# Performance work log

Measured on AMD Instinct MI355X. Metric: run time of the kernel, lower is better.

The kernel has to match this reference:

```python
import jax, jax.numpy as jnp
import numpy as np

B, S, D_IN, D_OUT, H = 2, 2048, 1024, 1024, 16
HD = D_OUT // H


def setup_inputs() -> dict:
    key = jax.random.key(0)
    ks = jax.random.split(key, 6)
    x = jax.random.normal(ks[0], (B, S, D_IN), jnp.float32)
    Wq = jax.random.normal(ks[1], (D_IN, D_OUT), jnp.float32) * 0.02
    Wk = jax.random.normal(ks[2], (D_IN, D_OUT), jnp.float32) * 0.02
    Wv = jax.random.normal(ks[3], (D_IN, D_OUT), jnp.float32) * 0.02
    Wo = jax.random.normal(ks[4], (D_OUT, D_OUT), jnp.float32) * 0.02
    bo = jax.random.normal(ks[5], (D_OUT,), jnp.float32) * 0.02
    return {"x": x, "Wq": Wq, "Wk": Wk, "Wv": Wv, "Wo": Wo, "bo": bo}


def reference(x, Wq, Wk, Wv, Wo, bo):
    b, s, _ = x.shape

    def to_heads(t):  # [b, s, d_out] -> [b, h, s, hd]
        return t.reshape(b, s, H, HD).transpose(0, 2, 1, 3)

    Q = to_heads(x @ Wq)
    K = to_heads(x @ Wk)
    V = to_heads(x @ Wv)

    scale = 1.0 / jnp.sqrt(jnp.asarray(HD, x.dtype))
    scores = jnp.einsum("bhqd,bhkd->bhqk", Q, K) * scale
    causal_mask = jnp.triu(jnp.ones((s, s), dtype=bool), k=1)  # True above diag
    scores = jnp.where(causal_mask, jnp.asarray(-1e6, scores.dtype), scores)
    weights = jax.nn.softmax(scores, axis=-1)  # dropout p=0.0 -> identity
    attn = jnp.einsum("bhqk,bhkd->bhqd", weights, V)  # [b, h, s, hd]
    # Faithful to source: reshape [b,h,s,hd] -> [b,s,d_out] WITHOUT head transpose-back
    attn = attn.reshape(b, s, D_OUT)
    return attn @ Wo + bo
```

## Files before the change

### kernel.cpp

```cpp
#include <hip/hip_runtime.h>
#include <stdint.h>


typedef unsigned short u16;
typedef __attribute__((ext_vector_type(8))) short bf16x8;
typedef __attribute__((ext_vector_type(4))) float f32x4;

#define MFMA_BF16(a, b, c) __builtin_amdgcn_mfma_f32_16x16x32_bf16((a), (b), (c), 0, 0, 0)
#define QSCALE 0.18033688011112042f

__device__ __forceinline__ u16 f2bf(float f) {
  union { float f; unsigned int u; } x; x.f = f;
  unsigned int r = x.u + 0x7fffu + ((x.u >> 16) & 1u);
  return (u16)(r >> 16);
}
__device__ __forceinline__ bf16x8 pack8(float4 a, float4 b) {
  bf16x8 r;
  r[0] = (short)f2bf(a.x); r[1] = (short)f2bf(a.y);
  r[2] = (short)f2bf(a.z); r[3] = (short)f2bf(a.w);
  r[4] = (short)f2bf(b.x); r[5] = (short)f2bf(b.y);
  r[6] = (short)f2bf(b.z); r[7] = (short)f2bf(b.w);
  return r;
}
__device__ __forceinline__ void gload_lds16(const u16* g, u16* l) {
  __builtin_amdgcn_global_load_lds((__attribute__((address_space(1))) void*)g,
                                   (__attribute__((address_space(3))) void*)l, 16, 0, 0);
}

template <int CPR>
__device__ __forceinline__ int sw_off(int r, int c) {
  return (r * CPR + (c ^ (r & (CPR - 1)))) * 8;
}

__global__ __launch_bounds__(256) void x_to_bf16(const float* __restrict__ x,
                                                 u16* __restrict__ xb) {
  const size_t i = ((size_t)blockIdx.x * 256 + threadIdx.x) * 8;
  const float4 a = *(const float4*)&x[i];
  const float4 b = *(const float4*)&x[i + 4];
  *(bf16x8*)&xb[i] = pack8(a, b);
}

__global__ void transpose_cols(const float* __restrict__ W0, const float* __restrict__ W1,
                               const float* __restrict__ W2, u16* __restrict__ T,
                               int h0, int hsx64) {
  __shared__ u16 t[32][33];
  const int j0 = blockIdx.x * 32;
  const int g = j0 / hsx64;
  const float* W = (g == 0) ? W0 : (g == 1) ? W1 : W2;
  const int wc0 = h0 * 64 + (j0 % hsx64);
  const int k0 = blockIdx.y * 32;
  t[threadIdx.y][threadIdx.x] =
      f2bf(W[(size_t)(k0 + threadIdx.y) * 1024 + wc0 + threadIdx.x]);
  __syncthreads();
  T[(size_t)(j0 + threadIdx.y) * 1024 + k0 + threadIdx.x] = t[threadIdx.x][threadIdx.y];
}

template <int MODE, int AF32>
__global__ __launch_bounds__(256, 2) void gemm_bt(
    const void* __restrict__ Av, const u16* __restrict__ BT,
    void* __restrict__ C0v, u16* __restrict__ C1, u16* __restrict__ C2,
    const float* __restrict__ bias, int M, int N, int K, int hs, int h0) {
  __shared__ __align__(16) u16 lsA[128 * 32];
  __shared__ __align__(16) u16 lsB[128 * 32];
  const int tid = threadIdx.x, lane = tid & 63, wv = tid >> 6;
  const int quad = lane >> 4, l16 = lane & 15;
  const int m0 = blockIdx.y * 128, n0 = blockIdx.x * 128;
  const int wm = (wv >> 1) * 64, wn = (wv & 1) * 64;
  const int hs64 = hs * 64;
  f32x4 acc[4][4] = {};

  for (int k0 = 0; k0 < K; k0 += 32) {
    if constexpr (AF32) {
      bf16x8 va[2], vb[2];
#pragma unroll
      for (int c = 0; c < 2; ++c) {
        const int P = c * 256 + tid, r = P >> 2, cc = P & 3;
        const float* Af = (const float*)Av;
        const float4 a0 = *(const float4*)&Af[(size_t)(m0 + r) * K + k0 + cc * 8];
        const float4 a1 = *(const float4*)&Af[(size_t)(m0 + r) * K + k0 + cc * 8 + 4];
        va[c] = pack8(a0, a1);
        vb[c] = *(const bf16x8*)&BT[(size_t)(n0 + r) * K + k0 + cc * 8];
      }
      __syncthreads();
#pragma unroll
      for (int c = 0; c < 2; ++c) {
        const int P = c * 256 + tid, r = P >> 2, cc = P & 3;
        *(bf16x8*)&lsA[sw_off<4>(r, cc)] = va[c];
        *(bf16x8*)&lsB[sw_off<4>(r, cc)] = vb[c];
      }
      __syncthreads();
    } else {
      __syncthreads();
#pragma unroll
      for (int c = 0; c < 2; ++c) {
        const int P = c * 256 + tid, r = P >> 2;
        const int gcol = ((P & 3) ^ (r & 3)) * 8;
        gload_lds16((const u16*)Av + (size_t)(m0 + r) * K + k0 + gcol,
                    &lsA[(size_t)(c * 256 + wv * 64) * 8]);
        gload_lds16(BT + (size_t)(n0 + r) * K + k0 + gcol,
                    &lsB[(size_t)(c * 256 + wv * 64) * 8]);
      }
      __syncthreads();
    }
    bf16x8 af[4], bfr[4];
#pragma unroll
    for (int i = 0; i < 4; ++i) af[i] = *(const bf16x8*)&lsA[sw_off<4>(wm + i * 16 + l16, quad)];
#pragma unroll
    for (int j = 0; j < 4; ++j) bfr[j] = *(const bf16x8*)&lsB[sw_off<4>(wn + j * 16 + l16, quad)];
#pragma unroll
    for (int i = 0; i < 4; ++i)
#pragma unroll
      for (int j = 0; j < 4; ++j) acc[i][j] = MFMA_BF16(af[i], bfr[j], acc[i][j]);
  }

#pragma unroll
  for (int i = 0; i < 4; ++i)
#pragma unroll
    for (int j = 0; j < 4; ++j) {
      const int n = n0 + wn + j * 16 + l16;
      float bv = 0.f;
      if constexpr (MODE == 1) bv = bias[n];
#pragma unroll
      for (int r = 0; r < 4; ++r) {
        const int m = m0 + wm + i * 16 + quad * 4 + r;
        if constexpr (MODE == 3) {
          const int b = m >> 11, s = m & 2047;
          if (n < hs64) {
            ((u16*)C0v)[((size_t)b * 2048 + s) * hs64 + n] = f2bf(acc[i][j][r] * QSCALE);
          } else if (n < 2 * hs64) {
            C1[((size_t)b * 2048 + s) * hs64 + (n - hs64)] = f2bf(acc[i][j][r]);
          } else {
            const int nn = n - 2 * hs64;
            C2[((size_t)(b * hs + (nn >> 6)) * 64 + (nn & 63)) * 2048 + s] =
                f2bf(acc[i][j][r]);
          }
        } else {
          const int b = (m >= hs * 128) ? 1 : 0;
          const int rp = m - b * hs * 128;
          ((float*)C0v)[(size_t)(b * 2048 + h0 * 128 + rp) * 1024 + n] =
              acc[i][j][r] + bv;
        }
      }
    }
}

__global__ __launch_bounds__(256, 2) void attn_fwd(
    const u16* __restrict__ Qsl, const u16* __restrict__ Ksl,
    const u16* __restrict__ VTsl, u16* __restrict__ A2sl, int hs) {
  __shared__ __align__(16) u16 lsK[2][64 * 64];
  __shared__ __align__(16) u16 lsV[2][64 * 64];
  __shared__ __align__(16) u16 lsP[4][16 * 64];
  __shared__ __align__(16) float scrl[64];
  const int tid = threadIdx.x, lane = tid & 63, wv = tid >> 6;
  const int quad = lane >> 4, l16 = lane & 15;
  const int grp = wv >> 1;
  const int wq = wv & 1;

  const int cpx = gridDim.x >> 3;
  const int w = (blockIdx.x & 7) * cpx + (blockIdx.x >> 3);
  const int bh = w >> 4;
  const int bx = w & 15;

  const int b = (bh >= hs) ? 1 : 0, hh = bh - b * hs;
  const int hs64 = hs * 64;
  const u16* Qb = Qsl + (size_t)b * 2048 * hs64;
  const u16* Kb = Ksl + (size_t)b * 2048 * hs64;
  const u16* Vb = VTsl + (size_t)(b * hs + hh) * 64 * 2048;
  u16* A2b = A2sl + (size_t)(b * hs + hh) * 2048 * 64;
  u16* lsPw = &lsP[wv][0];
  float* scro = (float*)&lsK[0][0];

  bf16x8 ones;
#pragma unroll
  for (int i = 0; i < 8; ++i) ones[i] = (short)0x3F80;

  const int prow = l16 >> 1;
  const int pb0 = (l16 & 1) << 2;

  for (int half = 0; half < 2; ++half) {
    const int qt = (half == 0) ? bx : 31 - bx;
    const int q0 = qt * 64;

    bf16x8 qf[2][2];
#pragma unroll
    for (int j = 0; j < 2; ++j)
#pragma unroll
      for (int ks = 0; ks < 2; ++ks)
        qf[j][ks] = *(const bf16x8*)&Qb[(size_t)(q0 + wq * 32 + j * 16 + l16) * hs64 +
                                        hh * 64 + ks * 32 + quad * 8];

    f32x4 acc_o[2][4] = {};
    f32x4 acc_l[2] = {};

    __syncthreads();
#pragma unroll
    for (int c = 0; c < 2; ++c) {
      const int P = c * 256 + tid;
      const int r = P >> 3, cc = (P & 7) ^ (r & 7);
      gload_lds16(Kb + (size_t)r * hs64 + hh * 64 + cc * 8,
                  &lsK[0][(c * 256 + wv * 64) * 8]);
      gload_lds16(Vb + (size_t)r * 2048 + cc * 8, &lsV[0][(c * 256 + wv * 64) * 8]);
    }

    for (int kt = 0; kt <= qt; ++kt) {
      const int k0 = kt * 64;
      const int buf = kt & 1;
      __syncthreads();
      if (kt < qt) {
        const int k1 = k0 + 64, nb = buf ^ 1;
#pragma unroll
        for (int c = 0; c < 2; ++c) {
          const int P = c * 256 + tid;
          const int r = P >> 3, cc = (P & 7) ^ (r & 7);
          gload_lds16(Kb + (size_t)(k1 + r) * hs64 + hh * 64 + cc * 8,
                      &lsK[nb][(c * 256 + wv * 64) * 8]);
          gload_lds16(Vb + (size_t)r * 2048 + k1 + cc * 8,
                      &lsV[nb][(c * 256 + wv * 64) * 8]);
        }
      }

      f32x4 accs[2][2] = {};
#pragma unroll
      for (int ks = 0; ks < 2; ++ks)
#pragma unroll
        for (int nj = 0; nj < 2; ++nj) {
          const bf16x8 kf = *(const bf16x8*)
              &lsK[buf][sw_off<8>(grp * 32 + nj * 16 + l16, ks * 4 + quad)];
          accs[0][nj] = MFMA_BF16(kf, qf[0][ks], accs[0][nj]);
          accs[1][nj] = MFMA_BF16(kf, qf[1][ks], accs[1][nj]);
        }

      const bool diag = (kt == qt);
#pragma unroll
      for (int j = 0; j < 2; ++j) {
        const int grow = q0 + wq * 32 + j * 16 + l16;
#pragma unroll
        for (int nj = 0; nj < 2; ++nj) {
          const int keyb = k0 + grp * 32 + nj * 16 + quad * 4;
#pragma unroll
          for (int r = 0; r < 4; ++r) {
            float p = exp2f(accs[j][nj][r]);
            if (diag) p = (keyb + r > grow) ? 0.f : p;
            accs[j][nj][r] = p;
          }
          union { float f; unsigned int u; } t0, t1, t2, t3;
          t0.f = accs[j][nj][0]; t1.f = accs[j][nj][1];
          t2.f = accs[j][nj][2]; t3.f = accs[j][nj][3];
          uint2 wpk;
          wpk.x = (t0.u >> 16) | (t1.u & 0xFFFF0000u);
          wpk.y = (t2.u >> 16) | (t3.u & 0xFFFF0000u);
          const int row = j * 8 + prow;
          const int chunk = (pb0 + 2 * nj + (quad >> 1)) ^ prow;
          *(uint2*)&lsPw[row * 64 + chunk * 8 + (quad & 1) * 4] = wpk;
        }
      }

      bf16x8 pf[2];
#pragma unroll
      for (int j = 0; j < 2; ++j) {
        const int row = j * 8 + prow;
        const int chunk = (pb0 + quad) ^ prow;
        pf[j] = *(const bf16x8*)&lsPw[row * 64 + chunk * 8];
        acc_l[j] = MFMA_BF16(ones, pf[j], acc_l[j]);
      }
#pragma unroll
      for (int njo = 0; njo < 4; ++njo) {
        const bf16x8 vf = *(const bf16x8*)
            &lsV[buf][sw_off<8>(njo * 16 + l16, grp * 4 + quad)];
        acc_o[0][njo] = MFMA_BF16(vf, pf[0], acc_o[0][njo]);
        acc_o[1][njo] = MFMA_BF16(vf, pf[1], acc_o[1][njo]);
      }
    }

    __syncthreads();
    if (grp == 1) {
#pragma unroll
      for (int j = 0; j < 2; ++j) {
#pragma unroll
        for (int njo = 0; njo < 4; ++njo) {
          const int ch = (njo * 4 + quad) ^ l16;
          *(f32x4*)&scro[(size_t)(wq * 32 + j * 16 + l16) * 64 + ch * 4] =
              acc_o[j][njo];
        }
        if (quad == 0) scrl[wq * 32 + j * 16 + l16] = acc_l[j][0];
      }
    }
    __syncthreads();
    if (grp == 0) {
#pragma unroll
      for (int j = 0; j < 2; ++j) {
        const int ql = wq * 32 + j * 16 + l16;
        const float inv = 1.0f / (acc_l[j][0] + scrl[ql]);
#pragma unroll
        for (int njo = 0; njo < 4; ++njo) {
          const int ch = (njo * 4 + quad) ^ l16;
          const f32x4 ob = *(const f32x4*)&scro[(size_t)ql * 64 + ch * 4];
          uint2 o;
          o.x = (unsigned)f2bf((acc_o[j][njo][0] + ob[0]) * inv) |
                ((unsigned)f2bf((acc_o[j][njo][1] + ob[1]) * inv) << 16);
          o.y = (unsigned)f2bf((acc_o[j][njo][2] + ob[2]) * inv) |
                ((unsigned)f2bf((acc_o[j][njo][3] + ob[3]) * inv) << 16);
          *(uint2*)&A2b[(size_t)(q0 + ql) * 64 + njo * 16 + quad * 4] = o;
        }
      }
    }
  }
}

extern "C" void kernel_launch(void* const* d_in, const int* in_sizes, int n_in,
                              void* d_out, int out_size, void* d_ws, size_t ws_size,
                              hipStream_t stream) {
  (void)in_sizes; (void)n_in; (void)out_size;
  const float* x  = (const float*)d_in[0];
  const float* Wq = (const float*)d_in[1];
  const float* Wk = (const float*)d_in[2];
  const float* Wv = (const float*)d_in[3];
  const float* Wo = (const float*)d_in[4];
  const float* bo = (const float*)d_in[5];
  float* out = (float*)d_out;
  char* ws = (char*)d_ws;
  const size_t MB = 1024 * 1024;
  const size_t KB = 1024;

  int hs = 2;
  if      (ws_size >= 2 * MB + 16 * 2432 * KB) hs = 16;
  else if (ws_size >= 2 * MB +  8 * 2432 * KB) hs = 8;
  else if (ws_size >= 2 * MB +  4 * 2432 * KB) hs = 4;

  u16* WoT   = (u16*)(ws);
  u16* Ksl   = (u16*)(ws + 2 * MB);
  u16* VTsl  = (u16*)(ws + 2 * MB + (size_t)hs *  512 * KB);
  u16* A2sl  = (u16*)(ws + 2 * MB + (size_t)hs * 1024 * KB);
  u16* WT3sl = (u16*)(ws + 2 * MB + (size_t)hs * 1536 * KB);
  u16* Qsl   = (u16*)(ws + 2 * MB + (size_t)hs * 1920 * KB);

  transpose_cols<<<dim3(32, 32), dim3(32, 32), 0, stream>>>(Wo, Wo, Wo, WoT, 0, 1024);
  if (hs == 16) {
    u16* xb = A2sl;
    x_to_bf16<<<2048, 256, 0, stream>>>(x, xb);
    transpose_cols<<<dim3(96, 32), dim3(32, 32), 0, stream>>>(Wq, Wk, Wv, WT3sl, 0, 1024);
    gemm_bt<3, 0><<<dim3(24, 32), 256, 0, stream>>>(
        (const void*)xb, WT3sl, (void*)Qsl, Ksl, VTsl, nullptr, 4096, 3072, 1024, 16, 0);
    attn_fwd<<<dim3(512), 256, 0, stream>>>(Qsl, Ksl, VTsl, A2sl, 16);
    gemm_bt<1, 0><<<dim3(8, 32), 256, 0, stream>>>(
        (const void*)A2sl, WoT, (void*)out, nullptr, nullptr, bo, 4096, 1024, 1024, 16, 0);
  } else {
    for (int h0 = 0; h0 < 16; h0 += hs) {
      transpose_cols<<<dim3(6 * hs, 32), dim3(32, 32), 0, stream>>>(Wq, Wk, Wv, WT3sl, h0, hs * 64);
      gemm_bt<3, 1><<<dim3((3 * hs) / 2, 32), 256, 0, stream>>>(
          (const void*)x, WT3sl, (void*)Qsl, Ksl, VTsl, nullptr, 4096, 3 * hs * 64, 1024, hs, h0);
      attn_fwd<<<dim3(16 * 2 * hs), 256, 0, stream>>>(Qsl, Ksl, VTsl, A2sl, hs);
      gemm_bt<1, 0><<<dim3(8, 2 * hs), 256, 0, stream>>>(
          (const void*)A2sl, WoT, (void*)out, nullptr, nullptr, bo, 2 * hs * 128, 1024, 1024, hs, h0);
    }
  }
}
```

Before: 198.2 us.

## Fuse prep kernels into one launch and peel the causal diagonal tile in attention

Merges the Wo transpose, the QKV weight transpose and the x-to-bf16 conversion into one prep kernel launch, which removes two launches and their serialization on the hs==16 path. In the attention kernel it precomputes the K/V global load pointers and advances them by a fixed stride on each tile. It also peels the diagonal tile out of the loop so the mask check runs only once, after the loop. This cuts per-iteration index arithmetic, and the peeled body duplicates code, which may add register pressure.

```diff
diff --git a/kernel.cpp b/kernel.cpp
--- a/kernel.cpp
+++ b/kernel.cpp
@@ -30,6 +30,41 @@
 template <int CPR>
 __device__ __forceinline__ int sw_off(int r, int c) {
   return (r * CPR + (c ^ (r & (CPR - 1)))) * 8;
+}
+
+__global__ __launch_bounds__(1024) void prep(
+    const float* __restrict__ x, u16* __restrict__ xb,
+    const float* __restrict__ Wq, const float* __restrict__ Wk,
+    const float* __restrict__ Wv, const float* __restrict__ Wo,
+    u16* __restrict__ WoT, u16* __restrict__ WT3) {
+  const int bxg = blockIdx.x, by = blockIdx.y;
+  if (bxg >= 128) {
+    const int blk = (bxg - 128) * 32 + by;
+    const int tid = threadIdx.y * 32 + threadIdx.x;
+    const size_t i = ((size_t)blk * 1024 + tid) * 8;
+    const float4 a = *(const float4*)&x[i];
+    const float4 b2 = *(const float4*)&x[i + 4];
+    *(bf16x8*)&xb[i] = pack8(a, b2);
+    return;
+  }
+  __shared__ u16 t[32][33];
+  const float* W;
+  u16* T;
+  int j0, wcol;
+  if (bxg < 32) {
+    j0 = bxg * 32; wcol = j0; W = Wo; T = WoT;
+  } else {
+    j0 = (bxg - 32) * 32;
+    const int g = j0 >> 10;
+    W = (g == 0) ? Wq : (g == 1) ? Wk : Wv;
+    T = WT3;
+    wcol = j0 & 1023;
+  }
+  const int k0 = by * 32;
+  t[threadIdx.y][threadIdx.x] =
+      f2bf(W[(size_t)(k0 + threadIdx.y) * 1024 + wcol + threadIdx.x]);
+  __syncthreads();
+  T[(size_t)(j0 + threadIdx.y) * 1024 + k0 + threadIdx.x] = t[threadIdx.x][threadIdx.y];
 }
 
 __global__ __launch_bounds__(256) void x_to_bf16(const float* __restrict__ x,
@@ -153,13 +188,11 @@
   __shared__ __align__(16) float scrl[64];
   const int tid = threadIdx.x, lane = tid & 63, wv = tid >> 6;
   const int quad = lane >> 4, l16 = lane & 15;
-  const int grp = wv >> 1;
-  const int wq = wv & 1;
+  const int grp = wv >> 1, wq = wv & 1;
 
   const int cpx = gridDim.x >> 3;
   const int w = (blockIdx.x & 7) * cpx + (blockIdx.x >> 3);
-  const int bh = w >> 4;
-  const int bx = w & 15;
+  const int bh = w >> 4, bx = w & 15;
 
   const int b = (bh >= hs) ? 1 : 0, hh = bh - b * hs;
   const int hs64 = hs * 64;
@@ -177,6 +210,16 @@
   const int prow = l16 >> 1;
   const int pb0 = (l16 & 1) << 2;
 
+  const int Pa = tid, ra = Pa >> 3, ca = (Pa & 7) ^ (ra & 7);
+  const int Pb2 = 256 + tid, rb = Pb2 >> 3, cb = (Pb2 & 7) ^ (rb & 7);
+  const size_t kTileStep = (size_t)64 * hs64;
+  const u16* const kBa = Kb + (size_t)ra * hs64 + hh * 64 + ca * 8;
+  const u16* const kBb = Kb + (size_t)rb * hs64 + hh * 64 + cb * 8;
+  const u16* const vBa = Vb + (size_t)ra * 2048 + ca * 8;
+  const u16* const vBb = Vb + (size_t)rb * 2048 + cb * 8;
+  const int dA = (wv * 64) * 8;
+  const int dB = (256 + wv * 64) * 8;
+
   for (int half = 0; half < 2; ++half) {
     const int qt = (half == 0) ? bx : 31 - bx;
     const int q0 = qt * 64;
@@ -192,33 +235,18 @@
     f32x4 acc_o[2][4] = {};
     f32x4 acc_l[2] = {};
 
+    const u16* pkA = kBa;
+    const u16* pkB = kBb;
+    const u16* pvA = vBa;
+    const u16* pvB = vBb;
+
     __syncthreads();
-#pragma unroll
-    for (int c = 0; c < 2; ++c) {
-      const int P = c * 256 + tid;
-      const int r = P >> 3, cc = (P & 7) ^ (r & 7);
-      gload_lds16(Kb + (size_t)r * hs64 + hh * 64 + cc * 8,
-                  &lsK[0][(c * 256 + wv * 64) * 8]);
-      gload_lds16(Vb + (size_t)r * 2048 + cc * 8, &lsV[0][(c * 256 + wv * 64) * 8]);
-    }
-
-    for (int kt = 0; kt <= qt; ++kt) {
-      const int k0 = kt * 64;
-      const int buf = kt & 1;
-      __syncthreads();
-      if (kt < qt) {
-        const int k1 = k0 + 64, nb = buf ^ 1;
-#pragma unroll
-        for (int c = 0; c < 2; ++c) {
-          const int P = c * 256 + tid;
-          const int r = P >> 3, cc = (P & 7) ^ (r & 7);
-          gload_lds16(Kb + (size_t)(k1 + r) * hs64 + hh * 64 + cc * 8,
-                      &lsK[nb][(c * 256 + wv * 64) * 8]);
-          gload_lds16(Vb + (size_t)r * 2048 + k1 + cc * 8,
-                      &lsV[nb][(c * 256 + wv * 64) * 8]);
-        }
-      }
-
+    gload_lds16(pkA, &lsK[0][dA]);
+    gload_lds16(pkB, &lsK[0][dB]);
+    gload_lds16(pvA, &lsV[0][dA]);
+    gload_lds16(pvB, &lsV[0][dB]);
+
+    auto body = [&](int buf, bool domask) {
       f32x4 accs[2][2] = {};
 #pragma unroll
       for (int ks = 0; ks < 2; ++ks)
@@ -229,18 +257,18 @@
           accs[0][nj] = MFMA_BF16(kf, qf[0][ks], accs[0][nj]);
           accs[1][nj] = MFMA_BF16(kf, qf[1][ks], accs[1][nj]);
         }
-
-      const bool diag = (kt == qt);
 #pragma unroll
       for (int j = 0; j < 2; ++j) {
-        const int grow = q0 + wq * 32 + j * 16 + l16;
+        const int grow = wq * 32 + j * 16 + l16;
 #pragma unroll
         for (int nj = 0; nj < 2; ++nj) {
-          const int keyb = k0 + grp * 32 + nj * 16 + quad * 4;
 #pragma unroll
           for (int r = 0; r < 4; ++r) {
             float p = exp2f(accs[j][nj][r]);
-            if (diag) p = (keyb + r > grow) ? 0.f : p;
+            if (domask) {
+              const int keyb = grp * 32 + nj * 16 + quad * 4;
+              p = (keyb + r > grow) ? 0.f : p;
+            }
             accs[j][nj][r] = p;
           }
           union { float f; unsigned int u; } t0, t1, t2, t3;
@@ -254,7 +282,6 @@
           *(uint2*)&lsPw[row * 64 + chunk * 8 + (quad & 1) * 4] = wpk;
         }
       }
-
       bf16x8 pf[2];
 #pragma unroll
       for (int j = 0; j < 2; ++j) {
@@ -270,6 +297,21 @@
         acc_o[0][njo] = MFMA_BF16(vf, pf[0], acc_o[0][njo]);
         acc_o[1][njo] = MFMA_BF16(vf, pf[1], acc_o[1][njo]);
       }
+    };
+
+    for (int kt = 0; kt < qt; ++kt) {
+      const int buf = kt & 1, nb = buf ^ 1;
+      __syncthreads();
+      pkA += kTileStep; pkB += kTileStep; pvA += 64; pvB += 64;
+      gload_lds16(pkA, &lsK[nb][dA]);
+      gload_lds16(pkB, &lsK[nb][dB]);
+      gload_lds16(pvA, &lsV[nb][dA]);
+      gload_lds16(pvB, &lsV[nb][dB]);
+      body(buf, false);
+    }
+    {
+      __syncthreads();
+      body(qt & 1, true);
     }
 
     __syncthreads();
@@ -334,17 +376,16 @@
   u16* WT3sl = (u16*)(ws + 2 * MB + (size_t)hs * 1536 * KB);
   u16* Qsl   = (u16*)(ws + 2 * MB + (size_t)hs * 1920 * KB);
 
-  transpose_cols<<<dim3(32, 32), dim3(32, 32), 0, stream>>>(Wo, Wo, Wo, WoT, 0, 1024);
   if (hs == 16) {
     u16* xb = A2sl;
-    x_to_bf16<<<2048, 256, 0, stream>>>(x, xb);
-    transpose_cols<<<dim3(96, 32), dim3(32, 32), 0, stream>>>(Wq, Wk, Wv, WT3sl, 0, 1024);
+    prep<<<dim3(144, 32), dim3(32, 32), 0, stream>>>(x, xb, Wq, Wk, Wv, Wo, WoT, WT3sl);
     gemm_bt<3, 0><<<dim3(24, 32), 256, 0, stream>>>(
         (const void*)xb, WT3sl, (void*)Qsl, Ksl, VTsl, nullptr, 4096, 3072, 1024, 16, 0);
     attn_fwd<<<dim3(512), 256, 0, stream>>>(Qsl, Ksl, VTsl, A2sl, 16);
     gemm_bt<1, 0><<<dim3(8, 32), 256, 0, stream>>>(
         (const void*)A2sl, WoT, (void*)out, nullptr, nullptr, bo, 4096, 1024, 1024, 16, 0);
   } else {
+    transpose_cols<<<dim3(32, 32), dim3(32, 32), 0, stream>>>(Wo, Wo, Wo, WoT, 0, 1024);
     for (int h0 = 0; h0 < 16; h0 += hs) {
       transpose_cols<<<dim3(6 * hs, 32), dim3(32, 32), 0, stream>>>(Wq, Wk, Wv, WT3sl, h0, hs * 64);
       gemm_bt<3, 1><<<dim3((3 * hs) / 2, 32), 256, 0, stream>>>(
```

After: 191.8 us. -3.3%, faster.
